# Optimization experiments

Measured on AMD Instinct MI355X. Metric: run time of the kernel, lower is better.

The kernel has to match this reference:

```python
import jax, jax.numpy as jnp
import numpy as np

N_NODES = 50000
N_EDGES = 800000
F_IN = 128
HID = 128
N_CLASSES = 16
N_GRAPHS = 64


def _glorot(key, shape):
    fan_in, fan_out = shape[0], shape[1]
    lim = (6.0 / (fan_in + fan_out)) ** 0.5
    return jax.random.uniform(key, shape, jnp.float32, -lim, lim)


def setup_inputs() -> dict:
    key = jax.random.key(0)
    ks = jax.random.split(key, 12)
    x = jax.random.normal(ks[0], (N_NODES, F_IN), jnp.float32)
    edge_index = jax.random.randint(ks[1], (2, N_EDGES), 0, N_NODES, jnp.int64)
    batch = jnp.sort(jax.random.randint(ks[2], (N_NODES,), 0, N_GRAPHS, jnp.int64))
    W0 = _glorot(ks[3], (F_IN, HID)); b0 = jnp.zeros((HID,), jnp.float32)
    W1 = _glorot(ks[4], (HID, HID)); b1 = jnp.zeros((HID,), jnp.float32)
    W2 = _glorot(ks[5], (HID, HID)); b2 = jnp.zeros((HID,), jnp.float32)
    Wc = _glorot(ks[6], (HID, N_CLASSES)); bc = jnp.zeros((N_CLASSES,), jnp.float32)
    return {"x": x, "edge_index": edge_index, "batch": batch,
            "W0": W0, "b0": b0, "W1": W1, "b1": b1, "W2": W2, "b2": b2,
            "Wc": Wc, "bc": bc}


def _gcn_prep(edge_index, n_nodes):
    # add self-loops, compute symmetric normalization coefficients
    loop = jnp.arange(n_nodes, dtype=edge_index.dtype)
    src = jnp.concatenate([edge_index[0], loop])
    dst = jnp.concatenate([edge_index[1], loop])
    deg = jax.ops.segment_sum(jnp.ones_like(dst, jnp.float32), dst, num_segments=n_nodes)
    dinv = deg ** -0.5  # deg >= 1 due to self-loops
    norm = dinv[src] * dinv[dst]  # [E+N]
    return src, dst, norm


def _gcn_layer(h, W, b, src, dst, norm, n_nodes):
    h = h @ W                                   # [N, out]
    msg = h[src] * norm[:, None]                # gather + scale [E+N, out]
    out = jax.ops.segment_sum(msg, dst, num_segments=n_nodes)  # scatter-add
    return out + b


def reference(x, edge_index, batch, W0, b0, W1, b1, W2, b2, Wc, bc):
    n = x.shape[0]
    src, dst, norm = _gcn_prep(edge_index, n)
    h = _gcn_layer(x, W0, b0, src, dst, norm, n)
    h = jax.nn.relu(h)  # dropout is identity in eval mode
    h = _gcn_layer(h, W1, b1, src, dst, norm, n)
    h = jax.nn.relu(h)
    h = _gcn_layer(h, W2, b2, src, dst, norm, n)
    # scatter-mean pooling over batch ids
    sums = jax.ops.segment_sum(h, batch, num_segments=N_GRAPHS)        # [G, HID]
    cnts = jax.ops.segment_sum(jnp.ones((n,), jnp.float32), batch, num_segments=N_GRAPHS)
    pooled = sums / jnp.maximum(cnts, 1.0)[:, None]
    return pooled @ Wc + bc  # [G, N_CLASSES]
```

## Files before the change

### kernel.cpp

```cpp
#include <hip/hip_runtime.h>
#include <hip/hip_bf16.h>
#include <hip/hip_fp16.h>

#define HID 128
#define NCLS 16
#define NGRAPH 64
#define CHUNK 1024

using bf16x8 = __attribute__((ext_vector_type(8))) short;
using f32x4  = __attribute__((ext_vector_type(4))) float;

__device__ __forceinline__ unsigned int f2bf(float f) {
    unsigned int u = __float_as_uint(f);
    return (u + 0x7FFFu + ((u >> 16) & 1u)) >> 16;
}
__device__ __forceinline__ float bf2f_lo(unsigned int u) { return __uint_as_float(u << 16); }
__device__ __forceinline__ float bf2f_hi(unsigned int u) { return __uint_as_float(u & 0xFFFF0000u); }

__global__ __launch_bounds__(256) void k_init(int* counts, float* pooled, float* cnt,
                                              const float* __restrict__ W0,
                                              const float* __restrict__ W1,
                                              unsigned short* __restrict__ Wt, int n) {
    int i = blockIdx.x * 256 + threadIdx.x;
    if (i < n) counts[i] = 0;
    if (i < NGRAPH * NCLS) pooled[i] = 0.0f;
    if (i < NGRAPH) cnt[i] = 0.0f;
    if (i < 2 * HID * HID) {
        int m = i >> 14;
        int r = i & 16383;
        int c = r >> 7, k = r & 127;
        const float* W = (m == 0) ? W0 : W1;
        Wt[i] = (unsigned short)f2bf(W[k * HID + c]);
    }
}

__global__ __launch_bounds__(256) void k_wc(const float* __restrict__ W2,
                                            const float* __restrict__ Wc,
                                            const float* __restrict__ b2,
                                            const float* __restrict__ bcin,
                                            unsigned short* __restrict__ Wt2c,
                                            float* __restrict__ bc2) {
    int tid = blockIdx.x * 256 + threadIdx.x;
    if (tid < HID * NCLS) {
        int k = tid >> 4, c = tid & 15;
        float s = 0.f;
        #pragma unroll 8
        for (int j = 0; j < HID; ++j)
            s = fmaf(W2[k * HID + j], Wc[j * NCLS + c], s);
        Wt2c[c * 128 + k] = (unsigned short)f2bf(s);
    }
    if (tid < NCLS) {
        float s = 0.f;
        for (int j = 0; j < HID; ++j)
            s = fmaf(b2[j], Wc[j * NCLS + tid], s);
        bc2[tid] = s + bcin[tid];
    }
}

__global__ __launch_bounds__(256) void k_hist(const int* __restrict__ dst,
                                              int* counts, int* rank, int e) {
    int i = blockIdx.x * 256 + threadIdx.x;
    if (i < e) rank[i] = atomicAdd(&counts[dst[i]], 1);
}

__global__ __launch_bounds__(256) void k_chunksum(const int* __restrict__ counts,
                                                  int* csum, int n) {
    __shared__ int sdata[256];
    int b = blockIdx.x, t = threadIdx.x;
    int base = b * CHUNK + t * 4;
    int s = 0;
    #pragma unroll
    for (int j = 0; j < 4; ++j) { int i = base + j; if (i < n) s += counts[i]; }
    sdata[t] = s; __syncthreads();
    for (int off = 128; off > 0; off >>= 1) {
        if (t < off) sdata[t] += sdata[t + off];
        __syncthreads();
    }
    if (t == 0) csum[b] = sdata[0];
}

__global__ __launch_bounds__(256) void k_rowptr(const int* __restrict__ counts,
                                                const int* __restrict__ csum,
                                                int* rowptr, int n, int e) {
    __shared__ int sincl[256];
    __shared__ int s_coff;
    int b = blockIdx.x, t = threadIdx.x;
    if (t < 64) {
        int v = (t < b) ? csum[t] : 0;
        #pragma unroll
        for (int off = 32; off > 0; off >>= 1) v += __shfl_xor(v, off);
        if (t == 0) s_coff = v;
    }
    int base = b * CHUNK + t * 4;
    int v[4]; int s = 0;
    #pragma unroll
    for (int j = 0; j < 4; ++j) { int i = base + j; v[j] = (i < n) ? counts[i] : 0; s += v[j]; }
    sincl[t] = s; __syncthreads();
    for (int off = 1; off < 256; off <<= 1) {
        int x = sincl[t];
        int y = (t >= off) ? sincl[t - off] : 0;
        __syncthreads();
        sincl[t] = x + y;
        __syncthreads();
    }
    int run = s_coff + sincl[t] - s;
    #pragma unroll
    for (int j = 0; j < 4; ++j) {
        int i = base + j;
        if (i < n) { rowptr[i] = run; run += v[j]; }
    }
    if (b == 0 && t == 0) rowptr[n] = e;
}

__global__ __launch_bounds__(256) void k_fill(const int* __restrict__ src,
                                              const int* __restrict__ dst,
                                              const int* __restrict__ rank,
                                              const int* __restrict__ counts,
                                              const int* __restrict__ rowptr,
                                              unsigned int* __restrict__ epk, int e) {
    int i = blockIdx.x * 256 + threadIdx.x;
    if (i >= e) return;
    int s = src[i], d = dst[i];
    int pos = rowptr[d] + rank[i];
    float norm = rsqrtf((float)(counts[s] + 1)) * rsqrtf((float)(counts[d] + 1));
    __half h = __float2half(norm);
    unsigned int hu = (unsigned int)__half_as_ushort(h);
    epk[pos] = (unsigned int)s | (hu << 16);
}

__global__ __launch_bounds__(256) void k_gemm_f32(const float* __restrict__ H,
                                                  const unsigned short* __restrict__ Wt,
                                                  unsigned short* __restrict__ Tb16, int n) {
    __shared__ char ldsA[64 * 256];
    int t = threadIdx.x;
    int cg = t & 31;
    int rg = t >> 5;
    int row0 = blockIdx.x * 64;

    #pragma unroll
    for (int i = 0; i < 8; ++i) {
        int lr = rg + i * 8;
        int r = row0 + lr;
        float4 v = make_float4(0.f, 0.f, 0.f, 0.f);
        if (r < n) v = ((const float4*)H)[(size_t)r * 32 + cg];
        uint2 pk;
        pk.x = f2bf(v.x) | (f2bf(v.y) << 16);
        pk.y = f2bf(v.z) | (f2bf(v.w) << 16);
        int byte = lr * 256 + cg * 8;
        *(uint2*)(ldsA + (byte ^ ((lr & 7) << 4))) = pk;
    }
    __syncthreads();

    int lane = t & 63;
    int w = t >> 6;
    int rsub = lane & 15;
    int kg = lane >> 4;
    int rowIdx = w * 16 + rsub;
    int abase = rowIdx * 256 + kg * 16;
    int aswz = (rowIdx & 7) << 4;

    f32x4 acc[8];
    #pragma unroll
    for (int nt = 0; nt < 8; ++nt) acc[nt] = (f32x4)(0.f);

    #pragma unroll
    for (int kk = 0; kk < 4; ++kk) {
        bf16x8 a = *(const bf16x8*)(ldsA + ((abase + kk * 64) ^ aswz));
        int k0 = kk * 32 + kg * 8;
        #pragma unroll
        for (int nt = 0; nt < 8; ++nt) {
            int col = nt * 16 + rsub;
            bf16x8 b = *(const bf16x8*)(Wt + col * 128 + k0);
            acc[nt] = __builtin_amdgcn_mfma_f32_16x16x32_bf16(a, b, acc[nt], 0, 0, 0);
        }
    }

    #pragma unroll
    for (int nt = 0; nt < 8; ++nt) {
        #pragma unroll
        for (int j = 0; j < 4; ++j) {
            int row = row0 + w * 16 + kg * 4 + j;
            int col = nt * 16 + rsub;
            if (row < n) Tb16[(size_t)row * 128 + col] = (unsigned short)f2bf(acc[nt][j]);
        }
    }
}

__global__ __launch_bounds__(256) void k_gemm_bf16(const unsigned short* __restrict__ Hb,
                                                   const unsigned short* __restrict__ Wt,
                                                   unsigned short* __restrict__ Tb16, int n) {
    __shared__ char ldsA[64 * 256];
    int t = threadIdx.x;
    int row0 = blockIdx.x * 64;
    int c16 = t & 15;
    int rbase = t >> 4;

    #pragma unroll
    for (int i = 0; i < 4; ++i) {
        int lr = rbase + i * 16;
        int r = row0 + lr;
        uint4 v = make_uint4(0u, 0u, 0u, 0u);
        if (r < n) v = *(const uint4*)(Hb + (size_t)r * 128 + c16 * 8);
        int byte = lr * 256 + c16 * 16;
        *(uint4*)(ldsA + (byte ^ ((lr & 7) << 4))) = v;
    }
    __syncthreads();

    int lane = t & 63;
    int w = t >> 6;
    int rsub = lane & 15;
    int kg = lane >> 4;
    int rowIdx = w * 16 + rsub;
    int abase = rowIdx * 256 + kg * 16;
    int aswz = (rowIdx & 7) << 4;

    f32x4 acc[8];
    #pragma unroll
    for (int nt = 0; nt < 8; ++nt) acc[nt] = (f32x4)(0.f);

    #pragma unroll
    for (int kk = 0; kk < 4; ++kk) {
        bf16x8 a = *(const bf16x8*)(ldsA + ((abase + kk * 64) ^ aswz));
        int k0 = kk * 32 + kg * 8;
        #pragma unroll
        for (int nt = 0; nt < 8; ++nt) {
            int col = nt * 16 + rsub;
            bf16x8 b = *(const bf16x8*)(Wt + col * 128 + k0);
            acc[nt] = __builtin_amdgcn_mfma_f32_16x16x32_bf16(a, b, acc[nt], 0, 0, 0);
        }
    }

    #pragma unroll
    for (int nt = 0; nt < 8; ++nt) {
        #pragma unroll
        for (int j = 0; j < 4; ++j) {
            int row = row0 + w * 16 + kg * 4 + j;
            int col = nt * 16 + rsub;
            if (row < n) Tb16[(size_t)row * 128 + col] = (unsigned short)f2bf(acc[nt][j]);
        }
    }
}

__global__ __launch_bounds__(256) void k_gemm16(const unsigned short* __restrict__ Hb,
                                                const unsigned short* __restrict__ Wt2c,
                                                float* __restrict__ T16, int n) {
    __shared__ char ldsA[64 * 256];
    int t = threadIdx.x;
    int row0 = blockIdx.x * 64;
    int c16 = t & 15;
    int rbase = t >> 4;

    #pragma unroll
    for (int i = 0; i < 4; ++i) {
        int lr = rbase + i * 16;
        int r = row0 + lr;
        uint4 v = make_uint4(0u, 0u, 0u, 0u);
        if (r < n) v = *(const uint4*)(Hb + (size_t)r * 128 + c16 * 8);
        int byte = lr * 256 + c16 * 16;
        *(uint4*)(ldsA + (byte ^ ((lr & 7) << 4))) = v;
    }
    __syncthreads();

    int lane = t & 63;
    int w = t >> 6;
    int rsub = lane & 15;
    int kg = lane >> 4;
    int rowIdx = w * 16 + rsub;
    int abase = rowIdx * 256 + kg * 16;
    int aswz = (rowIdx & 7) << 4;

    f32x4 acc = (f32x4)(0.f);
    #pragma unroll
    for (int kk = 0; kk < 4; ++kk) {
        bf16x8 a = *(const bf16x8*)(ldsA + ((abase + kk * 64) ^ aswz));
        int k0 = kk * 32 + kg * 8;
        bf16x8 b = *(const bf16x8*)(Wt2c + rsub * 128 + k0);
        acc = __builtin_amdgcn_mfma_f32_16x16x32_bf16(a, b, acc, 0, 0, 0);
    }

    #pragma unroll
    for (int j = 0; j < 4; ++j) {
        int row = row0 + w * 16 + kg * 4 + j;
        if (row < n) T16[(size_t)row * 16 + rsub] = acc[j];
    }
}

__global__ __launch_bounds__(256) void k_agg(const unsigned int* __restrict__ Tb,
                                             unsigned int* __restrict__ outB,
                                             const int* __restrict__ rowptr,
                                             const unsigned int* __restrict__ epk,
                                             const float* __restrict__ bias, int n) {
    int wid = (blockIdx.x * 256 + threadIdx.x) >> 6;
    int lane = threadIdx.x & 63;
    if (wid >= n) return;
    float2 b2 = ((const float2*)bias)[lane];
    unsigned int us = Tb[(size_t)wid * 64 + lane];
    int start = rowptr[wid];
    int deg = rowptr[wid + 1] - start;
    float sn = 1.0f / (float)(deg + 1);
    float2 acc;
    acc.x = fmaf(bf2f_lo(us), sn, b2.x);
    acc.y = fmaf(bf2f_hi(us), sn, b2.y);

    for (int j0 = 0; j0 < deg; j0 += 64) {
        int myj = j0 + lane;
        unsigned int rec = 0;
        if (myj < deg) rec = epk[start + myj];
        int m = min(64, deg - j0);
        int jj = 0;
        for (; jj + 16 <= m; jj += 16) {
            unsigned int rr[16], uu[16];
            #pragma unroll
            for (int k = 0; k < 16; ++k) rr[k] = (unsigned int)__shfl((int)rec, jj + k);
            #pragma unroll
            for (int k = 0; k < 16; ++k) uu[k] = Tb[(size_t)(rr[k] & 0xFFFFu) * 64 + lane];
            #pragma unroll
            for (int k = 0; k < 16; ++k) {
                float wk = __half2float(__ushort_as_half((unsigned short)(rr[k] >> 16)));
                acc.x = fmaf(wk, bf2f_lo(uu[k]), acc.x);
                acc.y = fmaf(wk, bf2f_hi(uu[k]), acc.y);
            }
        }
        for (; jj + 4 <= m; jj += 4) {
            unsigned int rr[4], uu[4];
            #pragma unroll
            for (int k = 0; k < 4; ++k) rr[k] = (unsigned int)__shfl((int)rec, jj + k);
            #pragma unroll
            for (int k = 0; k < 4; ++k) uu[k] = Tb[(size_t)(rr[k] & 0xFFFFu) * 64 + lane];
            #pragma unroll
            for (int k = 0; k < 4; ++k) {
                float wk = __half2float(__ushort_as_half((unsigned short)(rr[k] >> 16)));
                acc.x = fmaf(wk, bf2f_lo(uu[k]), acc.x);
                acc.y = fmaf(wk, bf2f_hi(uu[k]), acc.y);
            }
        }
        for (; jj < m; ++jj) {
            unsigned int rj = (unsigned int)__shfl((int)rec, jj);
            unsigned int u = Tb[(size_t)(rj & 0xFFFFu) * 64 + lane];
            float wj = __half2float(__ushort_as_half((unsigned short)(rj >> 16)));
            acc.x = fmaf(wj, bf2f_lo(u), acc.x);
            acc.y = fmaf(wj, bf2f_hi(u), acc.y);
        }
    }

    float rx = fmaxf(acc.x, 0.f), ry = fmaxf(acc.y, 0.f);
    outB[(size_t)wid * 64 + lane] = f2bf(rx) | (f2bf(ry) << 16);
}

__global__ __launch_bounds__(256) void k_agg16(const float* __restrict__ T16,
                                               float* __restrict__ G16,
                                               const int* __restrict__ rowptr,
                                               const unsigned int* __restrict__ epk, int n) {
    int wid = (blockIdx.x * 256 + threadIdx.x) >> 6;
    int lane = threadIdx.x & 63;
    if (wid >= n) return;
    int p = lane & 15;
    int q = lane >> 4;
    int start = rowptr[wid];
    int deg = rowptr[wid + 1] - start;

    float acc = 0.f;
    if (q == 0) {
        float sn = 1.0f / (float)(deg + 1);
        acc = T16[(size_t)wid * 16 + p] * sn;
    }

    for (int j0 = 0; j0 < deg; j0 += 64) {
        int myj = j0 + lane;
        unsigned int rec = 0;
        if (myj < deg) rec = epk[start + myj];
        int m = min(64, deg - j0);
        int mg = (m - q + 3) >> 2;
        int jj = 0;
        for (; jj + 8 <= mg; jj += 8) {
            unsigned int rr[8]; float uu[8];
            #pragma unroll
            for (int k = 0; k < 8; ++k) rr[k] = (unsigned int)__shfl((int)rec, 4 * (jj + k) + q);
            #pragma unroll
            for (int k = 0; k < 8; ++k) uu[k] = T16[(size_t)(rr[k] & 0xFFFFu) * 16 + p];
            #pragma unroll
            for (int k = 0; k < 8; ++k) {
                float wk = __half2float(__ushort_as_half((unsigned short)(rr[k] >> 16)));
                acc = fmaf(wk, uu[k], acc);
            }
        }
        for (; jj < mg; ++jj) {
            unsigned int rj = (unsigned int)__shfl((int)rec, 4 * jj + q);
            float u = T16[(size_t)(rj & 0xFFFFu) * 16 + p];
            float wj = __half2float(__ushort_as_half((unsigned short)(rj >> 16)));
            acc = fmaf(wj, u, acc);
        }
    }

    acc += __shfl_xor(acc, 16);
    acc += __shfl_xor(acc, 32);

    if (q == 0) G16[(size_t)wid * 16 + p] = acc;
}

__global__ __launch_bounds__(256) void k_pool16(const float* __restrict__ G16,
                                                const int* __restrict__ batch,
                                                float* pooled, float* cnt, int n) {
    int gw = (blockIdx.x * 256 + threadIdx.x) >> 6;
    int lane = threadIdx.x & 63;
    int p = lane & 15;
    int q = lane >> 4;
    int n0 = gw * 64;
    if (n0 >= n) return;
    int n1 = min(n0 + 64, n);
    int i0 = n0 + q;
    if (i0 >= n1) return;
    int gprev = batch[i0];
    float acc = 0.f;
    float runc = 0.f;
    for (int i = i0; i < n1; i += 4) {
        int g = batch[i];
        if (g != gprev) {
            atomicAdd(&pooled[gprev * NCLS + p], acc);
            if (p == 0) atomicAdd(&cnt[gprev], runc);
            acc = 0.f; runc = 0.f; gprev = g;
        }
        acc += G16[(size_t)i * 16 + p];
        runc += 1.f;
    }
    atomicAdd(&pooled[gprev * NCLS + p], acc);
    if (p == 0) atomicAdd(&cnt[gprev], runc);
}

__global__ __launch_bounds__(256) void k_head16(const float* __restrict__ pooled,
                                                const float* __restrict__ cnt,
                                                const float* __restrict__ bc2,
                                                float* __restrict__ out) {
    int idx = blockIdx.x * 256 + threadIdx.x;
    if (idx >= NGRAPH * NCLS) return;
    int g = idx >> 4, c = idx & 15;
    float inv = 1.0f / fmaxf(cnt[g], 1.0f);
    out[idx] = pooled[idx] * inv + bc2[c];
}

extern "C" void kernel_launch(void* const* d_in, const int* in_sizes, int n_in,
                              void* d_out, int out_size, void* d_ws, size_t ws_size,
                              hipStream_t stream) {
    const float* x    = (const float*)d_in[0];
    const int*   ei   = (const int*)d_in[1];
    const int*   batch= (const int*)d_in[2];
    const float* W0   = (const float*)d_in[3];
    const float* b0   = (const float*)d_in[4];
    const float* W1   = (const float*)d_in[5];
    const float* b1   = (const float*)d_in[6];
    const float* W2   = (const float*)d_in[7];
    const float* b2   = (const float*)d_in[8];
    const float* Wc   = (const float*)d_in[9];
    const float* bc   = (const float*)d_in[10];
    float* out = (float*)d_out;

    const int N = in_sizes[0] / HID;
    const int E = in_sizes[1] / 2;
    const int* src = ei;
    const int* dst = ei + E;

    char* p = (char*)d_ws;
    auto alloc = [&](size_t bytes) { void* r = (void*)p; p += (bytes + 255) & ~(size_t)255; return r; };
    int*   counts = (int*)alloc((size_t)N * 4);
    int*   rank   = (int*)alloc((size_t)E * 4);
    int*   csum   = (int*)alloc(256 * 4);
    int*   rowptr = (int*)alloc((size_t)(N + 1) * 4);
    unsigned int* epk = (unsigned int*)alloc((size_t)E * 4);
    float* pooled = (float*)alloc((size_t)NGRAPH * NCLS * 4);
    float* cnt    = (float*)alloc((size_t)NGRAPH * 4);
    unsigned short* Tb16 = (unsigned short*)alloc((size_t)N * HID * 2);
    unsigned short* Hb16 = (unsigned short*)alloc((size_t)N * HID * 2);
    float* T16    = (float*)alloc((size_t)N * NCLS * 4);
    float* G16    = (float*)alloc((size_t)N * NCLS * 4);
    unsigned short* Wt   = (unsigned short*)alloc((size_t)2 * HID * HID * 2);
    unsigned short* Wt2c = (unsigned short*)alloc((size_t)NCLS * 128 * 2);
    float* bc2    = (float*)alloc(NCLS * 4);

    const int NB = (N + CHUNK - 1) / CHUNK;

    k_init<<<(N + 255) / 256, 256, 0, stream>>>(counts, pooled, cnt, W0, W1, Wt, N);
    k_hist<<<(E + 255) / 256, 256, 0, stream>>>(dst, counts, rank, E);
    k_chunksum<<<NB, 256, 0, stream>>>(counts, csum, N);
    k_rowptr<<<NB, 256, 0, stream>>>(counts, csum, rowptr, N, E);
    k_fill<<<(E + 255) / 256, 256, 0, stream>>>(src, dst, rank, counts, rowptr, epk, E);
    k_wc<<<(HID * NCLS + 255) / 256, 256, 0, stream>>>(W2, Wc, b2, bc, Wt2c, bc2);

    const int gemm_grid = (N + 63) / 64;
    const int agg_grid  = ((size_t)N * 64 + 255) / 256;

    k_gemm_f32<<<gemm_grid, 256, 0, stream>>>(x, Wt, Tb16, N);
    k_agg<<<agg_grid, 256, 0, stream>>>((const unsigned int*)Tb16, (unsigned int*)Hb16,
                                        rowptr, epk, b0, N);
    k_gemm_bf16<<<gemm_grid, 256, 0, stream>>>(Hb16, Wt + 16384, Tb16, N);
    k_agg<<<agg_grid, 256, 0, stream>>>((const unsigned int*)Tb16, (unsigned int*)Hb16,
                                        rowptr, epk, b1, N);
    k_gemm16<<<gemm_grid, 256, 0, stream>>>(Hb16, Wt2c, T16, N);
    k_agg16<<<agg_grid, 256, 0, stream>>>(T16, G16, rowptr, epk, N);

    const int pool_blocks = (((N + 63) / 64) * 64 + 255) / 256;
    k_pool16<<<pool_blocks, 256, 0, stream>>>(G16, batch, pooled, cnt, N);
    k_head16<<<(NGRAPH * NCLS + 255) / 256, 256, 0, stream>>>(pooled, cnt, bc2, out);
}
```

Before: 236.8 us.

## Fuse second aggregation with class projection and pooling, merge setup kernels

Folds the weight-prep kernel into the init kernel and replaces the two-pass chunked scan with a single-block 1024-thread scan. Fuses layer-2 aggregation with the 128-to-16 projection in-kernel, and fuses the final 16-wide aggregation with graph pooling through atomics. Graph counts now come from binary search on the sorted batch ids. This drops several launches and the Hb16/G16 round trips, at the cost of a serial single-block scan and per-node atomics on pooled.

New measurement: 359.5 us. +51.8%, slower.

```diff
diff --git a/kernel.cpp b/kernel.cpp
--- a/kernel.cpp
+++ b/kernel.cpp
@@ -5,7 +5,6 @@
 #define HID 128
 #define NCLS 16
 #define NGRAPH 64
-#define CHUNK 1024
 
 using bf16x8 = __attribute__((ext_vector_type(8))) short;
 using f32x4  = __attribute__((ext_vector_type(4))) float;
@@ -17,14 +16,19 @@
 __device__ __forceinline__ float bf2f_lo(unsigned int u) { return __uint_as_float(u << 16); }
 __device__ __forceinline__ float bf2f_hi(unsigned int u) { return __uint_as_float(u & 0xFFFF0000u); }
 
-__global__ __launch_bounds__(256) void k_init(int* counts, float* pooled, float* cnt,
+__global__ __launch_bounds__(256) void k_init(int* counts, float* pooled,
                                               const float* __restrict__ W0,
                                               const float* __restrict__ W1,
-                                              unsigned short* __restrict__ Wt, int n) {
+                                              const float* __restrict__ W2,
+                                              const float* __restrict__ Wc,
+                                              const float* __restrict__ b2,
+                                              const float* __restrict__ bcin,
+                                              unsigned short* __restrict__ Wt,
+                                              unsigned short* __restrict__ Wt2c,
+                                              float* __restrict__ bc2, int n) {
     int i = blockIdx.x * 256 + threadIdx.x;
     if (i < n) counts[i] = 0;
     if (i < NGRAPH * NCLS) pooled[i] = 0.0f;
-    if (i < NGRAPH) cnt[i] = 0.0f;
     if (i < 2 * HID * HID) {
         int m = i >> 14;
         int r = i & 16383;
@@ -32,28 +36,19 @@
         const float* W = (m == 0) ? W0 : W1;
         Wt[i] = (unsigned short)f2bf(W[k * HID + c]);
     }
-}
-
-__global__ __launch_bounds__(256) void k_wc(const float* __restrict__ W2,
-                                            const float* __restrict__ Wc,
-                                            const float* __restrict__ b2,
-                                            const float* __restrict__ bcin,
-                                            unsigned short* __restrict__ Wt2c,
-                                            float* __restrict__ bc2) {
-    int tid = blockIdx.x * 256 + threadIdx.x;
-    if (tid < HID * NCLS) {
-        int k = tid >> 4, c = tid & 15;
+    if (i < HID * NCLS) {
+        int k = i >> 4, c = i & 15;
         float s = 0.f;
         #pragma unroll 8
         for (int j = 0; j < HID; ++j)
             s = fmaf(W2[k * HID + j], Wc[j * NCLS + c], s);
         Wt2c[c * 128 + k] = (unsigned short)f2bf(s);
     }
-    if (tid < NCLS) {
+    if (i < NCLS) {
         float s = 0.f;
         for (int j = 0; j < HID; ++j)
-            s = fmaf(b2[j], Wc[j * NCLS + tid], s);
-        bc2[tid] = s + bcin[tid];
+            s = fmaf(b2[j], Wc[j * NCLS + i], s);
+        bc2[i] = s + bcin[i];
     }
 }
 
@@ -63,53 +58,28 @@
     if (i < e) rank[i] = atomicAdd(&counts[dst[i]], 1);
 }
 
-__global__ __launch_bounds__(256) void k_chunksum(const int* __restrict__ counts,
-                                                  int* csum, int n) {
-    __shared__ int sdata[256];
-    int b = blockIdx.x, t = threadIdx.x;
-    int base = b * CHUNK + t * 4;
+__global__ __launch_bounds__(1024) void k_scan(const int* __restrict__ counts,
+                                               int* rowptr, int n, int e) {
+    __shared__ int sc[1024];
+    int t = threadIdx.x;
+    int per = (n + 1023) >> 10;
+    int base = t * per;
     int s = 0;
-    #pragma unroll
-    for (int j = 0; j < 4; ++j) { int i = base + j; if (i < n) s += counts[i]; }
-    sdata[t] = s; __syncthreads();
-    for (int off = 128; off > 0; off >>= 1) {
-        if (t < off) sdata[t] += sdata[t + off];
+    for (int j = 0; j < per; ++j) { int i = base + j; if (i < n) s += counts[i]; }
+    sc[t] = s; __syncthreads();
+    for (int off = 1; off < 1024; off <<= 1) {
+        int x = sc[t];
+        int y = (t >= off) ? sc[t - off] : 0;
         __syncthreads();
-    }
-    if (t == 0) csum[b] = sdata[0];
-}
-
-__global__ __launch_bounds__(256) void k_rowptr(const int* __restrict__ counts,
-                                                const int* __restrict__ csum,
-                                                int* rowptr, int n, int e) {
-    __shared__ int sincl[256];
-    __shared__ int s_coff;
-    int b = blockIdx.x, t = threadIdx.x;
-    if (t < 64) {
-        int v = (t < b) ? csum[t] : 0;
-        #pragma unroll
-        for (int off = 32; off > 0; off >>= 1) v += __shfl_xor(v, off);
-        if (t == 0) s_coff = v;
-    }
-    int base = b * CHUNK + t * 4;
-    int v[4]; int s = 0;
-    #pragma unroll
-    for (int j = 0; j < 4; ++j) { int i = base + j; v[j] = (i < n) ? counts[i] : 0; s += v[j]; }
-    sincl[t] = s; __syncthreads();
-    for (int off = 1; off < 256; off <<= 1) {
-        int x = sincl[t];
-        int y = (t >= off) ? sincl[t - off] : 0;
+        sc[t] = x + y;
         __syncthreads();
-        sincl[t] = x + y;
-        __syncthreads();
-    }
-    int run = s_coff + sincl[t] - s;
-    #pragma unroll
-    for (int j = 0; j < 4; ++j) {
+    }
+    int run = sc[t] - s;
+    for (int j = 0; j < per; ++j) {
         int i = base + j;
-        if (i < n) { rowptr[i] = run; run += v[j]; }
-    }
-    if (b == 0 && t == 0) rowptr[n] = e;
+        if (i < n) { rowptr[i] = run; run += counts[i]; }
+    }
+    if (t == 0) rowptr[n] = e;
 }
 
 __global__ __launch_bounds__(256) void k_fill(const int* __restrict__ src,
@@ -238,50 +208,6 @@
             int col = nt * 16 + rsub;
             if (row < n) Tb16[(size_t)row * 128 + col] = (unsigned short)f2bf(acc[nt][j]);
         }
-    }
-}
-
-__global__ __launch_bounds__(256) void k_gemm16(const unsigned short* __restrict__ Hb,
-                                                const unsigned short* __restrict__ Wt2c,
-                                                float* __restrict__ T16, int n) {
-    __shared__ char ldsA[64 * 256];
-    int t = threadIdx.x;
-    int row0 = blockIdx.x * 64;
-    int c16 = t & 15;
-    int rbase = t >> 4;
-
-    #pragma unroll
-    for (int i = 0; i < 4; ++i) {
-        int lr = rbase + i * 16;
-        int r = row0 + lr;
-        uint4 v = make_uint4(0u, 0u, 0u, 0u);
-        if (r < n) v = *(const uint4*)(Hb + (size_t)r * 128 + c16 * 8);
-        int byte = lr * 256 + c16 * 16;
-        *(uint4*)(ldsA + (byte ^ ((lr & 7) << 4))) = v;
-    }
-    __syncthreads();
-
-    int lane = t & 63;
-    int w = t >> 6;
-    int rsub = lane & 15;
-    int kg = lane >> 4;
-    int rowIdx = w * 16 + rsub;
-    int abase = rowIdx * 256 + kg * 16;
-    int aswz = (rowIdx & 7) << 4;
-
-    f32x4 acc = (f32x4)(0.f);
-    #pragma unroll
-    for (int kk = 0; kk < 4; ++kk) {
-        bf16x8 a = *(const bf16x8*)(ldsA + ((abase + kk * 64) ^ aswz));
-        int k0 = kk * 32 + kg * 8;
-        bf16x8 b = *(const bf16x8*)(Wt2c + rsub * 128 + k0);
-        acc = __builtin_amdgcn_mfma_f32_16x16x32_bf16(a, b, acc, 0, 0, 0);
-    }
-
-    #pragma unroll
-    for (int j = 0; j < 4; ++j) {
-        int row = row0 + w * 16 + kg * 4 + j;
-        if (row < n) T16[(size_t)row * 16 + rsub] = acc[j];
     }
 }
 
@@ -347,10 +273,103 @@
     outB[(size_t)wid * 64 + lane] = f2bf(rx) | (f2bf(ry) << 16);
 }
 
-__global__ __launch_bounds__(256) void k_agg16(const float* __restrict__ T16,
-                                               float* __restrict__ G16,
-                                               const int* __restrict__ rowptr,
-                                               const unsigned int* __restrict__ epk, int n) {
+__global__ __launch_bounds__(256) void k_agg_fused(const unsigned int* __restrict__ Tb,
+                                                   float* __restrict__ T16,
+                                                   const int* __restrict__ rowptr,
+                                                   const unsigned int* __restrict__ epk,
+                                                   const float* __restrict__ bias,
+                                                   const unsigned short* __restrict__ Wt2c,
+                                                   int n) {
+    __shared__ unsigned int sh[4][64];
+    int t = threadIdx.x;
+    int wid = (blockIdx.x * 256 + t) >> 6;
+    int lane = t & 63;
+    int w = t >> 6;
+    int c = lane & 15;
+    int half = lane >> 4;
+    bool valid = wid < n;
+
+    const uint4* wq = (const uint4*)((const unsigned int*)Wt2c + (c * 64 + half * 16));
+    uint4 wv0 = wq[0], wv1 = wq[1], wv2 = wq[2], wv3 = wq[3];
+    unsigned int wreg[16] = { wv0.x, wv0.y, wv0.z, wv0.w, wv1.x, wv1.y, wv1.z, wv1.w,
+                              wv2.x, wv2.y, wv2.z, wv2.w, wv3.x, wv3.y, wv3.z, wv3.w };
+
+    float2 acc = make_float2(0.f, 0.f);
+    int start = 0, deg = 0;
+    if (valid) {
+        float2 b2 = ((const float2*)bias)[lane];
+        unsigned int us = Tb[(size_t)wid * 64 + lane];
+        start = rowptr[wid];
+        deg = rowptr[wid + 1] - start;
+        float sn = 1.0f / (float)(deg + 1);
+        acc.x = fmaf(bf2f_lo(us), sn, b2.x);
+        acc.y = fmaf(bf2f_hi(us), sn, b2.y);
+    }
+
+    for (int j0 = 0; j0 < deg; j0 += 64) {
+        int myj = j0 + lane;
+        unsigned int rec = 0;
+        if (myj < deg) rec = epk[start + myj];
+        int m = min(64, deg - j0);
+        int jj = 0;
+        for (; jj + 16 <= m; jj += 16) {
+            unsigned int rr[16], uu[16];
+            #pragma unroll
+            for (int k = 0; k < 16; ++k) rr[k] = (unsigned int)__shfl((int)rec, jj + k);
+            #pragma unroll
+            for (int k = 0; k < 16; ++k) uu[k] = Tb[(size_t)(rr[k] & 0xFFFFu) * 64 + lane];
+            #pragma unroll
+            for (int k = 0; k < 16; ++k) {
+                float wk = __half2float(__ushort_as_half((unsigned short)(rr[k] >> 16)));
+                acc.x = fmaf(wk, bf2f_lo(uu[k]), acc.x);
+                acc.y = fmaf(wk, bf2f_hi(uu[k]), acc.y);
+            }
+        }
+        for (; jj + 4 <= m; jj += 4) {
+            unsigned int rr[4], uu[4];
+            #pragma unroll
+            for (int k = 0; k < 4; ++k) rr[k] = (unsigned int)__shfl((int)rec, jj + k);
+            #pragma unroll
+            for (int k = 0; k < 4; ++k) uu[k] = Tb[(size_t)(rr[k] & 0xFFFFu) * 64 + lane];
+            #pragma unroll
+            for (int k = 0; k < 4; ++k) {
+                float wk = __half2float(__ushort_as_half((unsigned short)(rr[k] >> 16)));
+                acc.x = fmaf(wk, bf2f_lo(uu[k]), acc.x);
+                acc.y = fmaf(wk, bf2f_hi(uu[k]), acc.y);
+            }
+        }
+        for (; jj < m; ++jj) {
+            unsigned int rj = (unsigned int)__shfl((int)rec, jj);
+            unsigned int u = Tb[(size_t)(rj & 0xFFFFu) * 64 + lane];
+            float wj = __half2float(__ushort_as_half((unsigned short)(rj >> 16)));
+            acc.x = fmaf(wj, bf2f_lo(u), acc.x);
+            acc.y = fmaf(wj, bf2f_hi(u), acc.y);
+        }
+    }
+
+    float rx = fmaxf(acc.x, 0.f), ry = fmaxf(acc.y, 0.f);
+    sh[w][lane] = f2bf(rx) | (f2bf(ry) << 16);
+    __syncthreads();
+
+    float part = 0.f;
+    #pragma unroll
+    for (int kk = 0; kk < 16; ++kk) {
+        unsigned int hu = sh[w][half * 16 + kk];
+        unsigned int wu = wreg[kk];
+        part = fmaf(bf2f_lo(hu), bf2f_lo(wu), part);
+        part = fmaf(bf2f_hi(hu), bf2f_hi(wu), part);
+    }
+    part += __shfl_xor(part, 16);
+    part += __shfl_xor(part, 32);
+
+    if (valid && half == 0) T16[(size_t)wid * 16 + c] = part;
+}
+
+__global__ __launch_bounds__(256) void k_agg16pool(const float* __restrict__ T16,
+                                                   float* __restrict__ pooled,
+                                                   const int* __restrict__ rowptr,
+                                                   const unsigned int* __restrict__ epk,
+                                                   const int* __restrict__ batch, int n) {
     int wid = (blockIdx.x * 256 + threadIdx.x) >> 6;
     int lane = threadIdx.x & 63;
     if (wid >= n) return;
@@ -395,46 +414,23 @@
     acc += __shfl_xor(acc, 16);
     acc += __shfl_xor(acc, 32);
 
-    if (q == 0) G16[(size_t)wid * 16 + p] = acc;
-}
-
-__global__ __launch_bounds__(256) void k_pool16(const float* __restrict__ G16,
+    if (q == 0) atomicAdd(&pooled[batch[wid] * NCLS + p], acc);
+}
+
+__global__ __launch_bounds__(256) void k_head16(const float* __restrict__ pooled,
                                                 const int* __restrict__ batch,
-                                                float* pooled, float* cnt, int n) {
-    int gw = (blockIdx.x * 256 + threadIdx.x) >> 6;
-    int lane = threadIdx.x & 63;
-    int p = lane & 15;
-    int q = lane >> 4;
-    int n0 = gw * 64;
-    if (n0 >= n) return;
-    int n1 = min(n0 + 64, n);
-    int i0 = n0 + q;
-    if (i0 >= n1) return;
-    int gprev = batch[i0];
-    float acc = 0.f;
-    float runc = 0.f;
-    for (int i = i0; i < n1; i += 4) {
-        int g = batch[i];
-        if (g != gprev) {
-            atomicAdd(&pooled[gprev * NCLS + p], acc);
-            if (p == 0) atomicAdd(&cnt[gprev], runc);
-            acc = 0.f; runc = 0.f; gprev = g;
-        }
-        acc += G16[(size_t)i * 16 + p];
-        runc += 1.f;
-    }
-    atomicAdd(&pooled[gprev * NCLS + p], acc);
-    if (p == 0) atomicAdd(&cnt[gprev], runc);
-}
-
-__global__ __launch_bounds__(256) void k_head16(const float* __restrict__ pooled,
-                                                const float* __restrict__ cnt,
                                                 const float* __restrict__ bc2,
-                                                float* __restrict__ out) {
+                                                float* __restrict__ out, int n) {
     int idx = blockIdx.x * 256 + threadIdx.x;
     if (idx >= NGRAPH * NCLS) return;
     int g = idx >> 4, c = idx & 15;
-    float inv = 1.0f / fmaxf(cnt[g], 1.0f);
+    int lo = 0, hi = n;
+    while (lo < hi) { int mid = (lo + hi) >> 1; if (batch[mid] < g) lo = mid + 1; else hi = mid; }
+    int lb = lo;
+    lo = 0; hi = n;
+    while (lo < hi) { int mid = (lo + hi) >> 1; if (batch[mid] < g + 1) lo = mid + 1; else hi = mid; }
+    float cnt = (float)(lo - lb);
+    float inv = 1.0f / fmaxf(cnt, 1.0f);
     out[idx] = pooled[idx] * inv + bc2[c];
 }
 
@@ -463,27 +459,21 @@
     auto alloc = [&](size_t bytes) { void* r = (void*)p; p += (bytes + 255) & ~(size_t)255; return r; };
     int*   counts = (int*)alloc((size_t)N * 4);
     int*   rank   = (int*)alloc((size_t)E * 4);
-    int*   csum   = (int*)alloc(256 * 4);
     int*   rowptr = (int*)alloc((size_t)(N + 1) * 4);
     unsigned int* epk = (unsigned int*)alloc((size_t)E * 4);
     float* pooled = (float*)alloc((size_t)NGRAPH * NCLS * 4);
-    float* cnt    = (float*)alloc((size_t)NGRAPH * 4);
     unsigned short* Tb16 = (unsigned short*)alloc((size_t)N * HID * 2);
     unsigned short* Hb16 = (unsigned short*)alloc((size_t)N * HID * 2);
     float* T16    = (float*)alloc((size_t)N * NCLS * 4);
-    float* G16    = (float*)alloc((size_t)N * NCLS * 4);
     unsigned short* Wt   = (unsigned short*)alloc((size_t)2 * HID * HID * 2);
     unsigned short* Wt2c = (unsigned short*)alloc((size_t)NCLS * 128 * 2);
     float* bc2    = (float*)alloc(NCLS * 4);
 
-    const int NB = (N + CHUNK - 1) / CHUNK;
-
-    k_init<<<(N + 255) / 256, 256, 0, stream>>>(counts, pooled, cnt, W0, W1, Wt, N);
+    k_init<<<(N + 255) / 256, 256, 0, stream>>>(counts, pooled, W0, W1, W2, Wc, b2, bc,
+                                                Wt, Wt2c, bc2, N);
     k_hist<<<(E + 255) / 256, 256, 0, stream>>>(dst, counts, rank, E);
-    k_chunksum<<<NB, 256, 0, stream>>>(counts, csum, N);
-    k_rowptr<<<NB, 256, 0, stream>>>(counts, csum, rowptr, N, E);
+    k_scan<<<1, 1024, 0, stream>>>(counts, rowptr, N, E);
     k_fill<<<(E + 255) / 256, 256, 0, stream>>>(src, dst, rank, counts, rowptr, epk, E);
-    k_wc<<<(HID * NCLS + 255) / 256, 256, 0, stream>>>(W2, Wc, b2, bc, Wt2c, bc2);
 
     const int gemm_grid = (N + 63) / 64;
     const int agg_grid  = ((size_t)N * 64 + 255) / 256;
@@ -492,12 +482,8 @@
     k_agg<<<agg_grid, 256, 0, stream>>>((const unsigned int*)Tb16, (unsigned int*)Hb16,
                                         rowptr, epk, b0, N);
     k_gemm_bf16<<<gemm_grid, 256, 0, stream>>>(Hb16, Wt + 16384, Tb16, N);
-    k_agg<<<agg_grid, 256, 0, stream>>>((const unsigned int*)Tb16, (unsigned int*)Hb16,
-                                        rowptr, epk, b1, N);
-    k_gemm16<<<gemm_grid, 256, 0, stream>>>(Hb16, Wt2c, T16, N);
-    k_agg16<<<agg_grid, 256, 0, stream>>>(T16, G16, rowptr, epk, N);
-
-    const int pool_blocks = (((N + 63) / 64) * 64 + 255) / 256;
-    k_pool16<<<pool_blocks, 256, 0, stream>>>(G16, batch, pooled, cnt, N);
-    k_head16<<<(NGRAPH * NCLS + 255) / 256, 256, 0, stream>>>(pooled, cnt, bc2, out);
-}
+    k_agg_fused<<<agg_grid, 256, 0, stream>>>((const unsigned int*)Tb16, T16,
+                                              rowptr, epk, b1, Wt2c, N);
+    k_agg16pool<<<agg_grid, 256, 0, stream>>>(T16, pooled, rowptr, epk, batch, N);
+    k_head16<<<(NGRAPH * NCLS + 255) / 256, 256, 0, stream>>>(pooled, batch, bc2, out, N);
+}
```
